# Performance work log

Hardware: AMD Instinct MI355X
Metric: run time of the kernel (lower is better)

The kernel has to match this reference:

```python
import jax, jax.numpy as jnp
import numpy as np

B, S, H = 4, 2048, 1024
E, K = 8, 2

def setup_inputs() -> dict:
    key = jax.random.key(0)
    ks = jax.random.split(key, 5)
    scale = 1.0 / np.sqrt(H)
    return {
        "x": jax.random.normal(ks[0], (B, S, H), dtype=jnp.float32),
        "router_w": jax.random.uniform(ks[1], (E, H), jnp.float32, -scale, scale),
        "router_b": jax.random.uniform(ks[2], (E,), jnp.float32, -scale, scale),
        "expert_w": jax.random.uniform(ks[3], (E, H, H), jnp.float32, -scale, scale),
        "expert_b": jax.random.uniform(ks[4], (E, H), jnp.float32, -scale, scale),
    }


def reference(x, router_w, router_b, expert_w, expert_b):
    # Router: [b,s,E]
    scores = jnp.einsum("bsh,eh->bse", x, router_w) + router_b
    probs = jax.nn.softmax(scores, axis=-1)
    p, expert_id = jax.lax.top_k(probs, K)          # [b,s,K]
    # Renormalize top-k probs (matches p / p.sum(dim=2))
    p = p / jnp.sum(p, axis=-1, keepdims=True)
    # Per-token combine weight per expert: [b,s,E]
    onehot = jax.nn.one_hot(expert_id, E, dtype=x.dtype)  # [b,s,K,E]
    w_comb = jnp.einsum("bske,bsk->bse", onehot, p)
    # All-expert linear (Linear: x @ W.T + b): [b,s,E,h]
    all_out = jnp.einsum("bsh,edh->bsed", x, expert_w) + expert_b
    # Weighted combine over selected experts: [b,s,h]
    return jnp.einsum("bse,bsed->bsd", w_comb, all_out)
```

## Files before the change

### kernel.cpp

```cpp
#include <hip/hip_runtime.h>
#include <hip/hip_bf16.h>
#include <math.h>

#define TOK 8192
#define HD 1024
#define NE 8
#define SLOTS 18432
#define NGRP 512
#define GRPSZ 16

typedef _Float16 half8 __attribute__((ext_vector_type(8)));
typedef _Float16 half4v __attribute__((ext_vector_type(4)));
typedef float floatx4 __attribute__((ext_vector_type(4)));

#define WAIT_VMCNT(N) asm volatile("s_waitcnt vmcnt(" #N ")" ::: "memory")
#define WAIT_LGKM0()  asm volatile("s_waitcnt lgkmcnt(0)" ::: "memory")
#define MEMFENCE()    asm volatile("" ::: "memory")

struct CTrue  { static constexpr bool value = true;  };
struct CFalse { static constexpr bool value = false; };

__global__ __launch_bounds__(256) void score_cvt(
    const float* __restrict__ x,
    const float* __restrict__ rw,
    const float* __restrict__ rb,
    const float* __restrict__ ew,
    _Float16* __restrict__ xh,
    _Float16* __restrict__ wh,
    int* __restrict__ epair,
    float* __restrict__ w1out,
    int* __restrict__ hist) {
  const int tid = threadIdx.x;
  const int blk = blockIdx.x;
  if (blk >= NGRP) {
    const int g = (blk - NGRP) * 256 + tid;
    const float4* src = (const float4*)ew;
    half4v* dst = (half4v*)wh;
#pragma unroll
    for (int j = 0; j < 4; ++j) {
      float4 v = src[g + 524288 * j];
      half4v h = {(_Float16)v.x, (_Float16)v.y, (_Float16)v.z, (_Float16)v.w};
      dst[g + 524288 * j] = h;
    }
    return;
  }
  const int lane = tid & 63;
  const int wid = tid >> 6;
  __shared__ int hcnt[NE];
  if (tid < NE) hcnt[tid] = 0;
  __syncthreads();

#pragma unroll
  for (int i = 0; i < 4; ++i) {
    const int t = blk * GRPSZ + wid * 4 + i;
    const float4* xp = (const float4*)(x + (size_t)t * HD);
    float4 xr[4];
#pragma unroll
    for (int k = 0; k < 4; ++k) xr[k] = xp[lane + 64 * k];
    _Float16* xo = xh + (size_t)t * HD;
#pragma unroll
    for (int k = 0; k < 4; ++k) {
      half4v h = {(_Float16)xr[k].x, (_Float16)xr[k].y,
                  (_Float16)xr[k].z, (_Float16)xr[k].w};
      *(half4v*)(xo + (lane + 64 * k) * 4) = h;
    }
    float sc[NE];
#pragma unroll
    for (int e = 0; e < NE; ++e) {
      const float4* wp = (const float4*)(rw + e * HD);
      float a = 0.f;
#pragma unroll
      for (int k = 0; k < 4; ++k) {
        float4 w = wp[lane + 64 * k];
        a += xr[k].x * w.x + xr[k].y * w.y + xr[k].z * w.z + xr[k].w * w.w;
      }
#pragma unroll
      for (int off = 32; off > 0; off >>= 1) a += __shfl_xor(a, off);
      sc[e] = a + rb[e];
    }
    float b1 = sc[0]; int e1 = 0;
#pragma unroll
    for (int e = 1; e < NE; ++e) if (sc[e] > b1) { b1 = sc[e]; e1 = e; }
    float b2 = -1e30f; int e2 = 0;
#pragma unroll
    for (int e = 0; e < NE; ++e) { if (e != e1 && sc[e] > b2) { b2 = sc[e]; e2 = e; } }
    if (lane == 0) {
      epair[t] = e1 | (e2 << 8);
      w1out[t] = 1.f / (1.f + expf(b2 - b1));
      atomicAdd(&hcnt[e1], 1);
      atomicAdd(&hcnt[e2], 1);
    }
  }
  __syncthreads();
  if (tid < NE) hist[tid * NGRP + blk] = hcnt[tid];
}

__global__ __launch_bounds__(256) void moe_scatter(
    const int* __restrict__ hist,
    const int* __restrict__ epair,
    const float* __restrict__ w1in,
    int* __restrict__ cntp,
    int* __restrict__ basep,
    int* __restrict__ tok_list,
    float* __restrict__ tok_w,
    int* __restrict__ slot_of) {
  const int tid = threadIdx.x;
  const int blk = blockIdx.x;
  __shared__ int pre_s[NE], tot_s[NE], alloc_s[NE];
  {
    const int e = tid >> 5;
    const int sl = tid & 31;
    int p = 0, tt = 0;
#pragma unroll
    for (int j = 0; j < 16; ++j) {
      int g = sl + 32 * j;
      int h = hist[e * NGRP + g];
      tt += h;
      p += (g < blk) ? h : 0;
    }
#pragma unroll
    for (int off = 16; off > 0; off >>= 1) {
      p += __shfl_xor(p, off);
      tt += __shfl_xor(tt, off);
    }
    if (sl == 0) { pre_s[e] = p; tot_s[e] = tt; }
  }
  __syncthreads();
  if (tid == 0) {
    int b = 0;
    for (int e = 0; e < NE; ++e) {
      alloc_s[e] = b + pre_s[e];
      if (blk == 0) { cntp[e * 64] = tot_s[e]; basep[e] = b; }
      b += (tot_s[e] + 255) & ~255;
    }
  }
  __syncthreads();
  if (tid < GRPSZ) {
    const int t = blk * GRPSZ + tid;
    int ep = epair[t];
    int e1 = ep & 0xff, e2 = ep >> 8;
    float w1 = w1in[t];
    int s1 = atomicAdd(&alloc_s[e1], 1);
    tok_list[s1] = t; tok_w[s1] = w1; slot_of[2 * t] = s1;
    int s2 = atomicAdd(&alloc_s[e2], 1);
    tok_list[s2] = t; tok_w[s2] = 1.f - w1; slot_of[2 * t + 1] = s2;
  }
}

template <int EPI>
__global__ __launch_bounds__(512, 2) void moe_gemm(
    const _Float16* __restrict__ Ah, const _Float16* __restrict__ Bh,
    const float* __restrict__ eb,
    const int* __restrict__ cntp, const int* __restrict__ base,
    const int* __restrict__ tok_list, const float* __restrict__ tok_w,
    _Float16* __restrict__ scratch, float* __restrict__ out) {
  const int ybl = blockIdx.y;
  const int e = ybl >> 5;
  const int mt = ybl & 31;
  const int ce = cntp[e * 64];
  const int m0 = mt << 8;
  if (m0 >= ce) return;
  const int nb = blockIdx.x << 8;
  const int sbase = base[e];
  const int tid = threadIdx.x;
  const int lane = tid & 63;
  const int wid = tid >> 6;
  const int wm = wid >> 2, wn = wid & 3;

  __shared__ _Float16 A_s[2][256 * 64];
  __shared__ _Float16 B_s[2][256 * 64];
  __shared__ int tok_s[256];
  __shared__ float w_s[256];

  if (tid < 256) {
    int tk = 0; float w = 0.f;
    if (m0 + tid < ce) { tk = tok_list[sbase + m0 + tid]; w = tok_w[sbase + m0 + tid]; }
    tok_s[tid] = tk; w_s[tid] = w;
  }
  __syncthreads();

  floatx4 acc[8][4];
  floatx4 zero = {0.f, 0.f, 0.f, 0.f};
#pragma unroll
  for (int i = 0; i < 8; ++i)
#pragma unroll
    for (int j = 0; j < 4; ++j) acc[i][j] = zero;

  const int wbase = e * HD * HD;
  const int rloc = lane >> 3, sub = lane & 7;
  const int g8 = (sub ^ rloc) * 8;
  int agoff[4], bgoff[4];
#pragma unroll
  for (int u = 0; u < 4; ++u) {
    const int row = (u >> 1) * 128 + wid * 16 + (u & 1) * 8 + rloc;
    agoff[u] = tok_s[row] * HD + g8;
    bgoff[u] = wbase + (nb + row) * HD + g8;
  }
  const int l15 = lane & 15, q4 = lane >> 4;
  const int ck0 = (q4 ^ (l15 & 7)) * 8;
  const int ck1 = ((4 + q4) ^ (l15 & 7)) * 8;

  auto gl = [](const _Float16* src, _Float16* dst) {
    __builtin_amdgcn_global_load_lds(
        (const __attribute__((address_space(1))) unsigned int*)src,
        (__attribute__((address_space(3))) unsigned int*)dst, 16, 0, 0);
  };
  auto stageA = [&](int uh, int buf, int k0) {
#pragma unroll
    for (int c = 0; c < 2; ++c) {
      const int r0 = uh * 128 + wid * 16 + c * 8;
      gl(Ah + agoff[uh * 2 + c] + k0, &A_s[buf][r0 * 64]);
    }
  };
  auto stageB = [&](int uh, int buf, int k0) {
#pragma unroll
    for (int c = 0; c < 2; ++c) {
      const int r0 = uh * 128 + wid * 16 + c * 8;
      gl(Bh + bgoff[uh * 2 + c] + k0, &B_s[buf][r0 * 64]);
    }
  };
  auto mf = [](half8 a, half8 b, floatx4 c) {
    return __builtin_amdgcn_mfma_f32_16x16x32_f16(a, b, c, 0, 0, 0);
  };

  stageA(0, 0, 0);
  stageB(0, 0, 0);
  stageB(1, 0, 0);
  stageA(1, 0, 0);

  auto run_tile = [&](int t, auto lastc) {
    constexpr bool LAST = decltype(lastc)::value;
    const int cur = t & 1, nxt = cur ^ 1;
    const int kn = (t + 1) * 64;
    half8 a0[4][2], a1[4][2], b01[2][2], b23[2][2];

    if constexpr (!LAST) { stageA(0, nxt, kn); WAIT_VMCNT(6); }
    else { WAIT_VMCNT(4); }
    __builtin_amdgcn_s_barrier();
    MEMFENCE();
#pragma unroll
    for (int i = 0; i < 4; ++i) {
      const int r = (wm * 64 + i * 16 + l15) * 64;
      a0[i][0] = *(const half8*)&A_s[cur][r + ck0];
      a0[i][1] = *(const half8*)&A_s[cur][r + ck1];
    }
#pragma unroll
    for (int j = 0; j < 2; ++j) {
      const int r = (wn * 32 + j * 16 + l15) * 64;
      b01[j][0] = *(const half8*)&B_s[cur][r + ck0];
      b01[j][1] = *(const half8*)&B_s[cur][r + ck1];
    }
    WAIT_LGKM0();
    __builtin_amdgcn_sched_barrier(0);
    __builtin_amdgcn_s_setprio(1);
#pragma unroll
    for (int i = 0; i < 4; ++i)
#pragma unroll
      for (int j = 0; j < 2; ++j) {
        acc[i][j] = mf(a0[i][0], b01[j][0], acc[i][j]);
        acc[i][j] = mf(a0[i][1], b01[j][1], acc[i][j]);
      }
    __builtin_amdgcn_s_setprio(0);

    if constexpr (!LAST) { stageB(0, nxt, kn); WAIT_VMCNT(6); }
    else { WAIT_VMCNT(2); }
    __builtin_amdgcn_s_barrier();
    MEMFENCE();
#pragma unroll
    for (int j = 0; j < 2; ++j) {
      const int r = (128 + wn * 32 + j * 16 + l15) * 64;
      b23[j][0] = *(const half8*)&B_s[cur][r + ck0];
      b23[j][1] = *(const half8*)&B_s[cur][r + ck1];
    }
    WAIT_LGKM0();
    __builtin_amdgcn_sched_barrier(0);
    __builtin_amdgcn_s_setprio(1);
#pragma unroll
    for (int i = 0; i < 4; ++i)
#pragma unroll
      for (int j = 0; j < 2; ++j) {
        acc[i][j + 2] = mf(a0[i][0], b23[j][0], acc[i][j + 2]);
        acc[i][j + 2] = mf(a0[i][1], b23[j][1], acc[i][j + 2]);
      }
    __builtin_amdgcn_s_setprio(0);

    if constexpr (!LAST) { stageB(1, nxt, kn); WAIT_VMCNT(6); }
    else { WAIT_VMCNT(0); }
    __builtin_amdgcn_s_barrier();
    MEMFENCE();
#pragma unroll
    for (int i = 0; i < 4; ++i) {
      const int r = (128 + wm * 64 + i * 16 + l15) * 64;
      a1[i][0] = *(const half8*)&A_s[cur][r + ck0];
      a1[i][1] = *(const half8*)&A_s[cur][r + ck1];
    }
    WAIT_LGKM0();
    __builtin_amdgcn_sched_barrier(0);
    __builtin_amdgcn_s_setprio(1);
#pragma unroll
    for (int i = 0; i < 4; ++i)
#pragma unroll
      for (int j = 0; j < 2; ++j) {
        acc[i + 4][j + 2] = mf(a1[i][0], b23[j][0], acc[i + 4][j + 2]);
        acc[i + 4][j + 2] = mf(a1[i][1], b23[j][1], acc[i + 4][j + 2]);
      }
    __builtin_amdgcn_s_setprio(0);

    if constexpr (!LAST) stageA(1, nxt, kn);
    __builtin_amdgcn_s_setprio(1);
#pragma unroll
    for (int i = 0; i < 4; ++i)
#pragma unroll
      for (int j = 0; j < 2; ++j) {
        acc[i + 4][j] = mf(a1[i][0], b01[j][0], acc[i + 4][j]);
        acc[i + 4][j] = mf(a1[i][1], b01[j][1], acc[i + 4][j]);
      }
    __builtin_amdgcn_s_setprio(0);
  };

  for (int t = 0; t < 15; ++t) run_tile(t, CFalse{});
  run_tile(15, CTrue{});

#pragma unroll
  for (int j = 0; j < 4; ++j) {
    const int col = nb + wn * 32 + (j & 1) * 16 + (j >> 1) * 128 + l15;
    const float bias = eb[e * HD + col];
#pragma unroll
    for (int i = 0; i < 8; ++i) {
      const int rbase = wm * 64 + (i & 3) * 16 + (i >> 2) * 128 + (q4 << 2);
#pragma unroll
      for (int r = 0; r < 4; ++r) {
        const int row = rbase + r;
        const float v = w_s[row] * (acc[i][j][r] + bias);
        if (EPI == 1) {
          scratch[(size_t)(sbase + m0 + row) * HD + col] = (_Float16)v;
        } else {
          if (m0 + row < ce)
            atomicAdd(&out[(size_t)tok_s[row] * HD + col], v);
        }
      }
    }
  }
}

__global__ void moe_combine(const _Float16* __restrict__ scratch,
                            const int* __restrict__ slot_of,
                            float* __restrict__ out) {
  const int tid = threadIdx.x;
  const int t = blockIdx.x * 2 + (tid >> 7);
  const int c = (tid & 127) * 8;
  int sa = slot_of[2 * t], sb = slot_of[2 * t + 1];
  half8 a = *(const half8*)&scratch[(size_t)sa * HD + c];
  half8 b = *(const half8*)&scratch[(size_t)sb * HD + c];
  float* o = out + (size_t)t * HD + c;
  float4 o0 = {(float)a[0] + (float)b[0], (float)a[1] + (float)b[1],
               (float)a[2] + (float)b[2], (float)a[3] + (float)b[3]};
  float4 o1 = {(float)a[4] + (float)b[4], (float)a[5] + (float)b[5],
               (float)a[6] + (float)b[6], (float)a[7] + (float)b[7]};
  *(float4*)o = o0;
  *(float4*)(o + 4) = o1;
}

extern "C" void kernel_launch(void* const* d_in, const int* in_sizes, int n_in,
                              void* d_out, int out_size, void* d_ws, size_t ws_size,
                              hipStream_t stream) {
  (void)in_sizes; (void)n_in;
  const float* x  = (const float*)d_in[0];
  const float* rw = (const float*)d_in[1];
  const float* rb = (const float*)d_in[2];
  const float* ew = (const float*)d_in[3];
  const float* eb = (const float*)d_in[4];
  float* out = (float*)d_out;

  char* w = (char*)d_ws;
  int*   cntp     = (int*)(w + 0);
  int*   basep    = (int*)(w + 2048);
  int*   hist     = (int*)(w + 2304);
  size_t off = 2304 + (size_t)NE * NGRP * 4;
  int*   tok_list = (int*)(w + off);  off += (size_t)SLOTS * 4;
  float* tok_w    = (float*)(w + off); off += (size_t)SLOTS * 4;
  int*   slot_of  = (int*)(w + off);  off += (size_t)TOK * 8;
  int*   epair    = (int*)(w + off);  off += (size_t)TOK * 4;
  float* w1buf    = (float*)(w + off); off += (size_t)TOK * 4;
  off = (off + 255) & ~255ull;
  size_t xh_off = off;
  size_t wh_off = xh_off + (size_t)TOK * HD * 2;
  size_t scr_off = wh_off + (size_t)NE * HD * HD * 2;
  size_t needscr = scr_off + (size_t)SLOTS * HD * 2;
  bool fastscr = ws_size >= needscr;

  if (!fastscr)
    hipMemsetAsync(d_out, 0, (size_t)out_size * sizeof(float), stream);

  _Float16* xh = (_Float16*)(w + xh_off);
  _Float16* wh = (_Float16*)(w + wh_off);
  _Float16* scr = fastscr ? (_Float16*)(w + scr_off) : nullptr;

  score_cvt<<<NGRP + 2048, 256, 0, stream>>>(x, rw, rb, ew, xh, wh,
                                             epair, w1buf, hist);
  moe_scatter<<<NGRP, 256, 0, stream>>>(hist, epair, w1buf, cntp, basep,
                                        tok_list, tok_w, slot_of);

  dim3 grid(HD / 256, NE * 32, 1);
  if (fastscr) {
    moe_gemm<1><<<grid, 512, 0, stream>>>(xh, wh, eb, cntp, basep,
                                          tok_list, tok_w, scr, out);
    moe_combine<<<TOK / 2, 256, 0, stream>>>(scr, slot_of, out);
  } else {
    moe_gemm<0><<<grid, 512, 0, stream>>>(xh, wh, eb, cntp, basep,
                                          tok_list, tok_w, nullptr, out);
  }
}
```

Before: 202.2 us.

## Reschedule GEMM prefetch after LDS reads and widen per-expert tile grid

Reorders the double-buffered K loop so each stage first reads its LDS fragments, then issues the next global-to-LDS prefetch, then synchronizes, with the vmcnt waits moved to the end of each phase. This lets the prefetch overlap the MFMA work instead of waiting before it. It also remaps which rows each wave stages into a strided 64-row interleave, and doubles the per-expert M-tile grid to 64. That covers experts holding more than 32×256 tokens at the cost of launching more blocks that exit early. The added barriers and removed sched_barriers risk extra sync overhead.

After: 196.7 us. -2.7%, faster.

```diff
diff --git a/kernel.cpp b/kernel.cpp
--- a/kernel.cpp
+++ b/kernel.cpp
@@ -154,9 +154,8 @@
     const int* __restrict__ cntp, const int* __restrict__ base,
     const int* __restrict__ tok_list, const float* __restrict__ tok_w,
     _Float16* __restrict__ scratch, float* __restrict__ out) {
-  const int ybl = blockIdx.y;
-  const int e = ybl >> 5;
-  const int mt = ybl & 31;
+  const int e = blockIdx.y >> 6;
+  const int mt = blockIdx.y & 63;
   const int ce = cntp[e * 64];
   const int m0 = mt << 8;
   if (m0 >= ce) return;
@@ -192,7 +191,7 @@
   int agoff[4], bgoff[4];
 #pragma unroll
   for (int u = 0; u < 4; ++u) {
-    const int row = (u >> 1) * 128 + wid * 16 + (u & 1) * 8 + rloc;
+    const int row = (u >> 1) * 128 + (u & 1) * 64 + wid * 8 + rloc;
     agoff[u] = tok_s[row] * HD + g8;
     bgoff[u] = wbase + (nb + row) * HD + g8;
   }
@@ -208,14 +207,14 @@
   auto stageA = [&](int uh, int buf, int k0) {
 #pragma unroll
     for (int c = 0; c < 2; ++c) {
-      const int r0 = uh * 128 + wid * 16 + c * 8;
+      const int r0 = uh * 128 + c * 64 + wid * 8;
       gl(Ah + agoff[uh * 2 + c] + k0, &A_s[buf][r0 * 64]);
     }
   };
   auto stageB = [&](int uh, int buf, int k0) {
 #pragma unroll
     for (int c = 0; c < 2; ++c) {
-      const int r0 = uh * 128 + wid * 16 + c * 8;
+      const int r0 = uh * 128 + c * 64 + wid * 8;
       gl(Bh + bgoff[uh * 2 + c] + k0, &B_s[buf][r0 * 64]);
     }
   };
@@ -227,6 +226,8 @@
   stageB(0, 0, 0);
   stageB(1, 0, 0);
   stageA(1, 0, 0);
+  WAIT_VMCNT(4);
+  __builtin_amdgcn_s_barrier();
 
   auto run_tile = [&](int t, auto lastc) {
     constexpr bool LAST = decltype(lastc)::value;
@@ -234,10 +235,6 @@
     const int kn = (t + 1) * 64;
     half8 a0[4][2], a1[4][2], b01[2][2], b23[2][2];
 
-    if constexpr (!LAST) { stageA(0, nxt, kn); WAIT_VMCNT(6); }
-    else { WAIT_VMCNT(4); }
-    __builtin_amdgcn_s_barrier();
-    MEMFENCE();
 #pragma unroll
     for (int i = 0; i < 4; ++i) {
       const int r = (wm * 64 + i * 16 + l15) * 64;
@@ -250,8 +247,10 @@
       b01[j][0] = *(const half8*)&B_s[cur][r + ck0];
       b01[j][1] = *(const half8*)&B_s[cur][r + ck1];
     }
+    if constexpr (!LAST) stageA(0, nxt, kn);
+    MEMFENCE();
+    __builtin_amdgcn_s_barrier();
     WAIT_LGKM0();
-    __builtin_amdgcn_sched_barrier(0);
     __builtin_amdgcn_s_setprio(1);
 #pragma unroll
     for (int i = 0; i < 4; ++i)
@@ -261,19 +260,19 @@
         acc[i][j] = mf(a0[i][1], b01[j][1], acc[i][j]);
       }
     __builtin_amdgcn_s_setprio(0);
-
-    if constexpr (!LAST) { stageB(0, nxt, kn); WAIT_VMCNT(6); }
-    else { WAIT_VMCNT(2); }
-    __builtin_amdgcn_s_barrier();
-    MEMFENCE();
+    if constexpr (!LAST) { WAIT_VMCNT(4); } else { WAIT_VMCNT(2); }
+    __builtin_amdgcn_s_barrier();
+
 #pragma unroll
     for (int j = 0; j < 2; ++j) {
       const int r = (128 + wn * 32 + j * 16 + l15) * 64;
       b23[j][0] = *(const half8*)&B_s[cur][r + ck0];
       b23[j][1] = *(const half8*)&B_s[cur][r + ck1];
     }
+    if constexpr (!LAST) stageB(0, nxt, kn);
+    MEMFENCE();
+    __builtin_amdgcn_s_barrier();
     WAIT_LGKM0();
-    __builtin_amdgcn_sched_barrier(0);
     __builtin_amdgcn_s_setprio(1);
 #pragma unroll
     for (int i = 0; i < 4; ++i)
@@ -283,19 +282,19 @@
         acc[i][j + 2] = mf(a0[i][1], b23[j][1], acc[i][j + 2]);
       }
     __builtin_amdgcn_s_setprio(0);
-
-    if constexpr (!LAST) { stageB(1, nxt, kn); WAIT_VMCNT(6); }
-    else { WAIT_VMCNT(0); }
-    __builtin_amdgcn_s_barrier();
-    MEMFENCE();
+    if constexpr (!LAST) { WAIT_VMCNT(4); } else { WAIT_VMCNT(0); }
+    __builtin_amdgcn_s_barrier();
+
 #pragma unroll
     for (int i = 0; i < 4; ++i) {
       const int r = (128 + wm * 64 + i * 16 + l15) * 64;
       a1[i][0] = *(const half8*)&A_s[cur][r + ck0];
       a1[i][1] = *(const half8*)&A_s[cur][r + ck1];
     }
+    if constexpr (!LAST) stageB(1, nxt, kn);
+    MEMFENCE();
+    __builtin_amdgcn_s_barrier();
     WAIT_LGKM0();
-    __builtin_amdgcn_sched_barrier(0);
     __builtin_amdgcn_s_setprio(1);
 #pragma unroll
     for (int i = 0; i < 4; ++i)
@@ -305,8 +304,10 @@
         acc[i + 4][j + 2] = mf(a1[i][1], b23[j][1], acc[i + 4][j + 2]);
       }
     __builtin_amdgcn_s_setprio(0);
+    __builtin_amdgcn_s_barrier();
 
     if constexpr (!LAST) stageA(1, nxt, kn);
+    MEMFENCE();
     __builtin_amdgcn_s_setprio(1);
 #pragma unroll
     for (int i = 0; i < 4; ++i)
@@ -316,6 +317,8 @@
         acc[i + 4][j] = mf(a1[i][1], b01[j][1], acc[i + 4][j]);
       }
     __builtin_amdgcn_s_setprio(0);
+    if constexpr (!LAST) WAIT_VMCNT(4);
+    __builtin_amdgcn_s_barrier();
   };
 
   for (int t = 0; t < 15; ++t) run_tile(t, CFalse{});
@@ -401,7 +404,7 @@
   moe_scatter<<<NGRP, 256, 0, stream>>>(hist, epair, w1buf, cntp, basep,
                                         tok_list, tok_w, slot_of);
 
-  dim3 grid(HD / 256, NE * 32, 1);
+  dim3 grid(HD / 256, NE * 64, 1);
   if (fastscr) {
     moe_gemm<1><<<grid, 512, 0, stream>>>(xh, wh, eb, cntp, basep,
                                           tok_list, tok_w, scr, out);
```
